# Performance work log

Hardware: AMD Instinct MI355X
Metric: run time of the kernel (lower is better)

## Reference

```python
import jax, jax.numpy as jnp
import numpy as np

EMBED_DIM = 1024
NUM_HEADS = 16
HEAD_DIM = EMBED_DIM // NUM_HEADS
LAMBDA_ENTANGLE = 0.35


def setup_inputs() -> dict:
    key = jax.random.key(0)
    ks = jax.random.split(key, 10)
    B, S, D = 2, 2048, EMBED_DIM
    init = 1.0 / np.sqrt(D)  # mimic nn.Linear uniform init scale
    x = jax.random.normal(ks[0], (B, S, D), dtype=jnp.float32)
    Wq = jax.random.uniform(ks[1], (D, D), jnp.float32, -init, init)
    bq = jax.random.uniform(ks[2], (D,), jnp.float32, -init, init)
    Wk = jax.random.uniform(ks[3], (D, D), jnp.float32, -init, init)
    bk = jax.random.uniform(ks[4], (D,), jnp.float32, -init, init)
    Wv = jax.random.uniform(ks[5], (D, D), jnp.float32, -init, init)
    bv = jax.random.uniform(ks[6], (D,), jnp.float32, -init, init)
    Wo = jax.random.uniform(ks[7], (D, D), jnp.float32, -init, init)
    bo = jax.random.uniform(ks[8], (D,), jnp.float32, -init, init)
    J_attn = jax.random.normal(ks[9], (NUM_HEADS, HEAD_DIM, HEAD_DIM), dtype=jnp.float32) * 0.02
    lambda_attn = jnp.asarray(LAMBDA_ENTANGLE, dtype=jnp.float32)
    return {"x": x, "Wq": Wq, "bq": bq, "Wk": Wk, "bk": bk, "Wv": Wv, "bv": bv,
            "Wo": Wo, "bo": bo, "J_attn": J_attn, "lambda_attn": lambda_attn}


def reference(x, Wq, bq, Wk, bk, Wv, bv, Wo, bo, J_attn, lambda_attn):
    B, S, D = x.shape
    H, Hd = NUM_HEADS, HEAD_DIM
    scale = jnp.sqrt(jnp.asarray(Hd, dtype=x.dtype))

    def heads(W, b):
        # (B,S,D) @ (D,D) + b -> (B,H,S,Hd)
        y = jnp.einsum('bsd,ed->bse', x, W) + b
        return y.reshape(B, S, H, Hd).transpose(0, 2, 1, 3)

    Q = heads(Wq, bq)
    K = heads(Wk, bk)
    V = heads(Wv, bv)

    scores = jnp.einsum('bhid,bhjd->bhij', Q, K) / scale
    # bilinear entanglement correction: tanh(Q) J tanh(K)^T
    QJ = jnp.einsum('bhid,hde->bhie', jnp.tanh(Q), J_attn)  # (B,H,S,Hd)
    delta = jnp.einsum('bhie,bhje->bhij', QJ, jnp.tanh(K))
    scores = scores + lambda_attn * delta

    causal = jnp.triu(jnp.ones((S, S), dtype=bool), k=1)
    scores = jnp.where(causal, -jnp.inf, scores)

    probs = jax.nn.softmax(scores, axis=-1)
    out = jnp.einsum('bhij,bhjd->bhid', probs, V)  # (B,H,S,Hd)
    out = out.transpose(0, 2, 1, 3).reshape(B, S, D)
    return jnp.einsum('bsd,ed->bse', out, Wo) + bo
```

## Files before the change

### kernel.cpp

```cpp
#include <hip/hip_runtime.h>
#include <hip/hip_bf16.h>

typedef unsigned short u16;
typedef __bf16 bf16x8 __attribute__((ext_vector_type(8)));
typedef float f32x4 __attribute__((ext_vector_type(4)));
typedef unsigned short u16x4 __attribute__((ext_vector_type(4)));

#define MFMA16(a, b, c) __builtin_amdgcn_mfma_f32_16x16x32_bf16(a, b, c, 0, 0, 0)

#define EMB 1024
#define SEQ 2048
#define NH 16
#define HD 64
#define LOG2E 1.4426950408889634f

#define GLOAD_LDS16(g, l) __builtin_amdgcn_global_load_lds( \
    (const __attribute__((address_space(1))) unsigned int*)(g), \
    (__attribute__((address_space(3))) unsigned int*)(l), 16, 0, 0)

__device__ __forceinline__ float b2f(u16 u) {
    union { unsigned int i; float f; } v; v.i = ((unsigned int)u) << 16; return v.f;
}
__device__ __forceinline__ u16 f2b(float f) {
    __hip_bfloat16 h = __float2bfloat16(f);
    return *reinterpret_cast<u16*>(&h);
}
__device__ __forceinline__ u16x4 pack4(float a, float b, float c, float d) {
    union { __hip_bfloat162 h2[2]; u16x4 u; } r;
    r.h2[0] = __float22bfloat162_rn(float2{a, b});
    r.h2[1] = __float22bfloat162_rn(float2{c, d});
    return r.u;
}
__device__ __forceinline__ bf16x8 ldfrag(const u16* p) {
    return *reinterpret_cast<const bf16x8*>(p);
}
__device__ __forceinline__ bf16x8 cvt8(const float* p) {
    const float4 a = *reinterpret_cast<const float4*>(p);
    const float4 b = *reinterpret_cast<const float4*>(p + 4);
    union { u16x4 q[2]; bf16x8 v; } r;
    r.q[0] = pack4(a.x, a.y, a.z, a.w);
    r.q[1] = pack4(b.x, b.y, b.z, b.w);
    return r.v;
}
__device__ __forceinline__ float fast_tanh(float x) {
    float t = __builtin_amdgcn_exp2f(x * (2.0f * LOG2E));
    return 1.0f - 2.0f * __builtin_amdgcn_rcpf(t + 1.0f);
}
__device__ __forceinline__ bf16x8 tanh8(bf16x8 v) {
    union { bf16x8 v; u16 u[8]; } in; in.v = v;
    float o[8];
#pragma unroll
    for (int e = 0; e < 8; e++) o[e] = fast_tanh(b2f(in.u[e]));
    union { u16x4 q[2]; bf16x8 v; } r;
    r.q[0] = pack4(o[0], o[1], o[2], o[3]);
    r.q[1] = pack4(o[4], o[5], o[6], o[7]);
    return r.v;
}

__global__ __launch_bounds__(256) void cvt_all(
        const float* __restrict__ x,  const float* __restrict__ Wq,
        const float* __restrict__ Wk, const float* __restrict__ Wv,
        const float* __restrict__ Wo, u16* __restrict__ dst)
{
    size_t i = ((size_t)blockIdx.x * 256 + threadIdx.x) * 8;
    const float* src; size_t off;
    if (i < 4194304) { src = x; off = i; }
    else {
        size_t j = i - 4194304; int w = (int)(j >> 20); off = j & 1048575;
        src = (w == 0) ? Wq : (w == 1) ? Wk : (w == 2) ? Wv : Wo;
    }
    *(bf16x8*)&dst[i] = cvt8(src + off);
}

template<int MI>
__global__ __launch_bounds__(256, 4) void gemm_epi(
        const u16* __restrict__ A,
        const u16* __restrict__ W0, const float* __restrict__ B0,
        const u16* __restrict__ W1, const float* __restrict__ B1,
        const u16* __restrict__ W2, const float* __restrict__ B2,
        const float* __restrict__ lam,
        u16* __restrict__ Qa, u16* __restrict__ Ka, u16* __restrict__ Vt,
        float* __restrict__ out, int modeBase)
{
    const int mode = modeBase + blockIdx.z;
    const u16* W; const float* bias;
    if (blockIdx.z == 0)      { W = W0; bias = B0; }
    else if (blockIdx.z == 1) { W = W1; bias = B1; }
    else                      { W = W2; bias = B2; }

    __shared__ __attribute__((aligned(16))) u16 sA[MI * 32 * 64];
    __shared__ __attribute__((aligned(16))) u16 sB[128 * 64];

    const int t = threadIdx.x;
    const int w = t >> 6, L = t & 63;
    const int wm = w >> 1, wn = w & 1;
    const int lr = L & 15, lq = L >> 4;
    const int wbase = t & 192;
    const int m0 = blockIdx.y * (MI * 32), n0 = blockIdx.x * 128;

    f32x4 acc[MI][4];
#pragma unroll
    for (int i = 0; i < MI; i++)
#pragma unroll
        for (int j = 0; j < 4; j++) { f32x4 z = {0.f, 0.f, 0.f, 0.f}; acc[i][j] = z; }

    for (int k0 = 0; k0 < EMB; k0 += 64) {
        __syncthreads();
#pragma unroll
        for (int q = 0; q < MI; q++) {
            int c = q * 256 + t;
            int row = c >> 3, cc = c & 7;
            int col8 = cc ^ (row & 7);
            GLOAD_LDS16(&A[(size_t)(m0 + row) * EMB + k0 + col8 * 8],
                        &sA[(q * 256 + wbase) * 8]);
        }
#pragma unroll
        for (int q = 0; q < 4; q++) {
            int c = q * 256 + t;
            int row = c >> 3, cc = c & 7;
            int col8 = cc ^ (row & 7);
            GLOAD_LDS16(&W[(size_t)(n0 + row) * EMB + k0 + col8 * 8],
                        &sB[(q * 256 + wbase) * 8]);
        }
        __syncthreads();
#pragma unroll
        for (int s = 0; s < 2; s++) {
            bf16x8 af[MI], bfr[4];
#pragma unroll
            for (int mi = 0; mi < MI; mi++) {
                int row = wm * (MI * 16) + mi * 16 + lr;
                af[mi] = ldfrag(&sA[(row * 8 + ((s * 4 + lq) ^ (row & 7))) * 8]);
            }
#pragma unroll
            for (int ni = 0; ni < 4; ni++) {
                int row = wn * 64 + ni * 16 + lr;
                bfr[ni] = ldfrag(&sB[(row * 8 + ((s * 4 + lq) ^ (row & 7))) * 8]);
            }
#pragma unroll
            for (int mi = 0; mi < MI; mi++)
#pragma unroll
                for (int ni = 0; ni < 4; ni++)
                    acc[mi][ni] = MFMA16(af[mi], bfr[ni], acc[mi][ni]);
        }
    }

    const float lamf = lam[0];
#pragma unroll
    for (int mi = 0; mi < MI; mi++)
#pragma unroll
        for (int ni = 0; ni < 4; ni++) {
            int mb = m0 + wm * (MI * 16) + mi * 16 + lq * 4;
            int n  = n0 + wn * 64 + ni * 16 + lr;
            float bv = bias[n];
            if (mode == 3) {
#pragma unroll
                for (int r = 0; r < 4; r++)
                    out[(size_t)(mb + r) * EMB + n] = acc[mi][ni][r] + bv;
            } else {
                int b = mb >> 11, s0 = mb & 2047;
                int h = n >> 6,  d = n & 63;
                if (mode == 0) {
#pragma unroll
                    for (int r = 0; r < 4; r++) {
                        float val = acc[mi][ni][r] + bv;
                        size_t i128 = ((size_t)(b * NH + h) * SEQ + s0 + r) * 128 + d;
                        Qa[i128]      = f2b(val * (0.125f * LOG2E));
                        Qa[i128 + 64] = f2b(lamf * LOG2E * fast_tanh(val));
                    }
                } else if (mode == 1) {
#pragma unroll
                    for (int r = 0; r < 4; r++) {
                        float val = acc[mi][ni][r] + bv;
                        Ka[((size_t)(b * NH + h) * SEQ + s0 + r) * 128 + d] = f2b(val);
                    }
                } else {
                    u16x4 pk = pack4(acc[mi][ni][0] + bv, acc[mi][ni][1] + bv,
                                     acc[mi][ni][2] + bv, acc[mi][ni][3] + bv);
                    *(u16x4*)&Vt[((size_t)(b * NH + h) * HD + d) * SEQ + s0] = pk;
                }
            }
        }
}

__global__ __launch_bounds__(256) void ukern(
        const float* __restrict__ J, u16* __restrict__ Ka)
{
    __shared__ __attribute__((aligned(16))) u16 sJ[64 * 72];
    const int t = threadIdx.x, w = t >> 6, L = t & 63, lr = L & 15, lq = L >> 4;
    const int rt = blockIdx.x, bh = blockIdx.y, h = bh & 15;

#pragma unroll
    for (int i = 0; i < 2; i++) {
        int c = t + 256 * i;
        int row = c >> 3, col = (c & 7) * 8;
        *(bf16x8*)&sJ[row * 72 + col] = cvt8(&J[(size_t)h * 4096 + row * 64 + col]);
    }
    __syncthreads();

    const u16* krow = &Ka[((size_t)bh * SEQ + rt * 64 + w * 16 + lr) * 128];
    bf16x8 a0 = tanh8(ldfrag(krow + lq * 8));
    bf16x8 a1 = tanh8(ldfrag(krow + lq * 8 + 32));
#pragma unroll
    for (int nt = 0; nt < 4; nt++) {
        f32x4 acc = {0.f, 0.f, 0.f, 0.f};
        acc = MFMA16(a0, ldfrag(&sJ[(nt * 16 + lr) * 72 + lq * 8]), acc);
        acc = MFMA16(a1, ldfrag(&sJ[(nt * 16 + lr) * 72 + lq * 8 + 32]), acc);
#pragma unroll
        for (int r = 0; r < 4; r++) {
            int j = rt * 64 + w * 16 + lq * 4 + r;
            Ka[((size_t)bh * SEQ + j) * 128 + 64 + nt * 16 + lr] = f2b(acc[r]);
        }
    }
}

__global__ __launch_bounds__(512) void flash(
        const u16* __restrict__ Qa, const u16* __restrict__ Ka,
        const u16* __restrict__ Vt, u16* __restrict__ attn)
{
    __shared__ __attribute__((aligned(16))) u16 sK[2][64 * 128];
    __shared__ __attribute__((aligned(16))) u16 sVt[2][64 * 64];
    __shared__ __attribute__((aligned(16))) u16 sP[128 * 72];
    __shared__ float sLs[2][4][64][2];

    const int t = threadIdx.x, w = t >> 6, L = t & 63, lr = L & 15, lq = L >> 4;
    const int wq = w & 3, wk = w >> 2;
    const int bh = blockIdx.x & 31, p = blockIdx.x >> 5;
    const int i_l = wq * 16 + lr;
    const u16* Kbase = Ka + (size_t)bh * SEQ * 128;
    const u16* Vbase = Vt + (size_t)bh * HD * SEQ;
    const int b = bh >> 4, h = bh & 15;
    float* sOt = reinterpret_cast<float*>(sK);

    const int kr0 = t >> 4,        kc0 = (t & 15) ^ (kr0 & 15);
    const int kr1 = (512 + t) >> 4, kc1 = (t & 15) ^ (kr1 & 15);
    const int vd = t >> 3,          vj8 = (t & 7) ^ (vd & 7);
    const u16* kq0 = Kbase + (size_t)kr0 * 128 + kc0 * 8;
    const u16* kq1 = Kbase + (size_t)kr1 * 128 + kc1 * 8;
    const u16* vq  = Vbase + (size_t)vd * SEQ + vj8 * 8;

#pragma unroll 1
    for (int seg = 0; seg < 2; seg++) {
        const int qt = seg ? 15 - p : p;
        const int qm = qt * 128;
        const int ktmax = 2 * qt + 1;

        bf16x8 qf[2][4];
#pragma unroll
        for (int g = 0; g < 2; g++) {
            const u16* qrow = Qa + ((size_t)bh * SEQ + qm + g * 64 + i_l) * 128;
#pragma unroll
            for (int s = 0; s < 4; s++) qf[g][s] = ldfrag(qrow + s * 32 + lq * 8);
        }

        f32x4 Ot[2][4];
#pragma unroll
        for (int g = 0; g < 2; g++)
#pragma unroll
            for (int i = 0; i < 4; i++) { f32x4 z = {0.f, 0.f, 0.f, 0.f}; Ot[g][i] = z; }
        float lsum[2] = {0.f, 0.f};

        {
            int4 rk0 = *(const int4*)kq0;
            int4 rk1 = *(const int4*)kq1;
            int4 rv  = *(const int4*)vq;
            *(int4*)&sK[0][(size_t)t * 8]         = rk0;
            *(int4*)&sK[0][(size_t)(512 + t) * 8] = rk1;
            *(int4*)&sVt[0][(size_t)t * 8]        = rv;
        }
        __syncthreads();

        int cur = 0;
        for (int kt = 0; kt <= ktmax; kt++) {
            const bool pf = kt < ktmax;
            int4 rk0, rk1, rv;
            if (pf) {
                const int kn = (kt + 1) * 64;
                rk0 = *(const int4*)(kq0 + (size_t)kn * 128);
                rk1 = *(const int4*)(kq1 + (size_t)kn * 128);
                rv  = *(const int4*)(vq + kn);
            }
            const u16* sKc = sK[cur];
            const u16* sVc = sVt[cur];

            f32x4 sc[2][2];
#pragma unroll
            for (int g = 0; g < 2; g++)
#pragma unroll
                for (int m = 0; m < 2; m++) { f32x4 z = {0.f,0.f,0.f,0.f}; sc[g][m] = z; }
            __builtin_amdgcn_s_setprio(1);
#pragma unroll
            for (int mt2 = 0; mt2 < 2; mt2++) {
                int j = (wk * 2 + mt2) * 16 + lr;
#pragma unroll
                for (int s = 0; s < 4; s++) {
                    bf16x8 kf = ldfrag(&sKc[(j * 16 + ((s * 4 + lq) ^ (j & 15))) * 8]);
                    sc[0][mt2] = MFMA16(kf, qf[0][s], sc[0][mt2]);
                    sc[1][mt2] = MFMA16(kf, qf[1][s], sc[1][mt2]);
                }
            }
            __builtin_amdgcn_s_setprio(0);
            if (kt >= ktmax - 1) {
                const int thr0 = (kt == ktmax) ? -1  : i_l;
                const int thr1 = (kt == ktmax) ? i_l : 63;
#pragma unroll
                for (int mt2 = 0; mt2 < 2; mt2++)
#pragma unroll
                    for (int r = 0; r < 4; r++) {
                        int j = (wk * 2 + mt2) * 16 + lq * 4 + r;
                        if (j > thr0) sc[0][mt2][r] = -INFINITY;
                        if (j > thr1) sc[1][mt2][r] = -INFINITY;
                    }
            }
#pragma unroll
            for (int g = 0; g < 2; g++) {
#pragma unroll
                for (int mt2 = 0; mt2 < 2; mt2++) {
                    float e0 = __builtin_amdgcn_exp2f(sc[g][mt2][0]);
                    float e1 = __builtin_amdgcn_exp2f(sc[g][mt2][1]);
                    float e2 = __builtin_amdgcn_exp2f(sc[g][mt2][2]);
                    float e3 = __builtin_amdgcn_exp2f(sc[g][mt2][3]);
                    lsum[g] += (e0 + e1) + (e2 + e3);
                    *(u16x4*)&sP[(g * 64 + i_l) * 72 + (wk * 2 + mt2) * 16 + lq * 4] =
                        pack4(e0, e1, e2, e3);
                }
            }
            __builtin_amdgcn_s_setprio(1);
            {
                bf16x8 pf0 = ldfrag(&sP[(i_l) * 72 + wk * 32 + lq * 8]);
                bf16x8 pf1 = ldfrag(&sP[(64 + i_l) * 72 + wk * 32 + lq * 8]);
#pragma unroll
                for (int mt = 0; mt < 4; mt++) {
                    int d = mt * 16 + lr;
                    bf16x8 vf = ldfrag(&sVc[(d * 8 + ((wk * 4 + lq) ^ (d & 7))) * 8]);
                    Ot[0][mt] = MFMA16(vf, pf0, Ot[0][mt]);
                    Ot[1][mt] = MFMA16(vf, pf1, Ot[1][mt]);
                }
            }
            __builtin_amdgcn_s_setprio(0);
            if (pf) {
                *(int4*)&sK[cur ^ 1][(size_t)t * 8]         = rk0;
                *(int4*)&sK[cur ^ 1][(size_t)(512 + t) * 8] = rk1;
                *(int4*)&sVt[cur ^ 1][(size_t)t * 8]        = rv;
            }
            __syncthreads();
            cur ^= 1;
        }

#pragma unroll
        for (int g = 0; g < 2; g++) {
            lsum[g] += __shfl_xor(lsum[g], 16);
            lsum[g] += __shfl_xor(lsum[g], 32);
            sLs[wk][wq][L][g] = lsum[g];
        }
        if (wk == 1) {
            float* dst = &sOt[wq * 64 + L];
#pragma unroll
            for (int g = 0; g < 2; g++)
#pragma unroll
                for (int mt = 0; mt < 4; mt++)
#pragma unroll
                    for (int r = 0; r < 4; r++)
                        dst[256 * (g * 16 + mt * 4 + r)] = Ot[g][mt][r];
        }
        __syncthreads();
        if (wk == 0) {
            const float* src = &sOt[wq * 64 + L];
#pragma unroll
            for (int g = 0; g < 2; g++) {
                float ls = lsum[g] + sLs[1][wq][L][g];
                const float r0 = __builtin_amdgcn_rcpf(ls);
                const float inv = r0 * (2.0f - ls * r0);
                const size_t base =
                    ((size_t)(b * SEQ + qm + g * 64 + i_l)) * EMB + h * HD;
#pragma unroll
                for (int mt = 0; mt < 4; mt++)
                    *(u16x4*)&attn[base + mt * 16 + lq * 4] = pack4(
                        (Ot[g][mt][0] + src[256 * (g * 16 + mt * 4 + 0)]) * inv,
                        (Ot[g][mt][1] + src[256 * (g * 16 + mt * 4 + 1)]) * inv,
                        (Ot[g][mt][2] + src[256 * (g * 16 + mt * 4 + 2)]) * inv,
                        (Ot[g][mt][3] + src[256 * (g * 16 + mt * 4 + 3)]) * inv);
            }
        }
        __syncthreads();
    }
}

extern "C" void kernel_launch(void* const* d_in, const int* in_sizes, int n_in,
                              void* d_out, int out_size, void* d_ws, size_t ws_size,
                              hipStream_t stream)
{
    const float* x   = (const float*)d_in[0];
    const float* Wq  = (const float*)d_in[1];
    const float* bq  = (const float*)d_in[2];
    const float* Wk  = (const float*)d_in[3];
    const float* bk  = (const float*)d_in[4];
    const float* Wv  = (const float*)d_in[5];
    const float* bv  = (const float*)d_in[6];
    const float* Wo  = (const float*)d_in[7];
    const float* bo  = (const float*)d_in[8];
    const float* J   = (const float*)d_in[9];
    const float* lam = (const float*)d_in[10];

    u16* ws  = (u16*)d_ws;
    u16* xb  = ws;
    u16* Wqb = xb  + (size_t)4096 * 1024;
    u16* Wkb = Wqb + (size_t)1024 * 1024;
    u16* Wvb = Wkb + (size_t)1024 * 1024;
    u16* Wob = Wvb + (size_t)1024 * 1024;
    u16* Qa  = Wob + (size_t)1024 * 1024;
    u16* Ka  = Qa  + (size_t)32 * 2048 * 128;
    u16* Vt  = Ka  + (size_t)32 * 2048 * 128;
    u16* attn = xb;
    float* dout = (float*)d_out;

    dim3 blk(256);
    cvt_all<<<dim3(4096), blk, 0, stream>>>(x, Wq, Wk, Wv, Wo, ws);
    gemm_epi<4><<<dim3(8, 32, 3), blk, 0, stream>>>(
        xb, Wqb, bq, Wkb, bk, Wvb, bv, lam, Qa, Ka, Vt, dout, 0);
    ukern<<<dim3(32, 32), blk, 0, stream>>>(J, Ka);
    flash<<<dim3(256), dim3(512), 0, stream>>>(Qa, Ka, Vt, attn);
    gemm_epi<2><<<dim3(8, 64, 1), blk, 0, stream>>>(
        attn, Wob, bo, Wob, bo, Wob, bo, lam, Qa, Ka, Vt, dout, 3);
}
```

Before: 190.8 us.

## Fuse tanh(K)·J into K projection epilogue and enlarge flash KV tile

The separate ukern launch is removed. The K-projection GEMM epilogue now stages tanh(K) in its shared memory and multiplies it by a bf16 copy of J, which cvt_all now produces. Separately, the flash attention kernel's key/value tile grows from 64 to 128 columns, halving loop iterations and barriers, and the causal masking logic is simplified to match. The cost is much larger LDS use in flash (double-buffered 128-row K/V plus a wider P tile), which may lower occupancy, and an extra barrier plus MFMA work in the K GEMM blocks.

```diff
diff --git a/kernel.cpp b/kernel.cpp
--- a/kernel.cpp
+++ b/kernel.cpp
@@ -46,30 +46,24 @@
     float t = __builtin_amdgcn_exp2f(x * (2.0f * LOG2E));
     return 1.0f - 2.0f * __builtin_amdgcn_rcpf(t + 1.0f);
 }
-__device__ __forceinline__ bf16x8 tanh8(bf16x8 v) {
-    union { bf16x8 v; u16 u[8]; } in; in.v = v;
-    float o[8];
-#pragma unroll
-    for (int e = 0; e < 8; e++) o[e] = fast_tanh(b2f(in.u[e]));
-    union { u16x4 q[2]; bf16x8 v; } r;
-    r.q[0] = pack4(o[0], o[1], o[2], o[3]);
-    r.q[1] = pack4(o[4], o[5], o[6], o[7]);
-    return r.v;
-}
 
 __global__ __launch_bounds__(256) void cvt_all(
         const float* __restrict__ x,  const float* __restrict__ Wq,
         const float* __restrict__ Wk, const float* __restrict__ Wv,
-        const float* __restrict__ Wo, u16* __restrict__ dst)
+        const float* __restrict__ Wo, const float* __restrict__ J,
+        u16* __restrict__ dst)
 {
     size_t i = ((size_t)blockIdx.x * 256 + threadIdx.x) * 8;
-    const float* src; size_t off;
-    if (i < 4194304) { src = x; off = i; }
-    else {
+    const float* src; size_t off; u16* d;
+    if (i < 4194304) { src = x; off = i; d = dst + i; }
+    else if (i < 8388608) {
         size_t j = i - 4194304; int w = (int)(j >> 20); off = j & 1048575;
         src = (w == 0) ? Wq : (w == 1) ? Wk : (w == 2) ? Wv : Wo;
-    }
-    *(bf16x8*)&dst[i] = cvt8(src + off);
+        d = dst + i;
+    } else {
+        off = i - 8388608; src = J; d = dst + 29360128 + off;
+    }
+    *(bf16x8*)d = cvt8(src + off);
 }
 
 template<int MI>
@@ -78,7 +72,7 @@
         const u16* __restrict__ W0, const float* __restrict__ B0,
         const u16* __restrict__ W1, const float* __restrict__ B1,
         const u16* __restrict__ W2, const float* __restrict__ B2,
-        const float* __restrict__ lam,
+        const float* __restrict__ lam, const u16* __restrict__ Jb,
         u16* __restrict__ Qa, u16* __restrict__ Ka, u16* __restrict__ Vt,
         float* __restrict__ out, int modeBase)
 {
@@ -144,6 +138,9 @@
         }
     }
 
+    if (mode == 1) __syncthreads();
+    u16* sU = (w < 2) ? &sA[(size_t)w * 4096] : &sB[(size_t)(w - 2) * 4096];
+
     const float lamf = lam[0];
 #pragma unroll
     for (int mi = 0; mi < MI; mi++)
@@ -172,6 +169,9 @@
                     for (int r = 0; r < 4; r++) {
                         float val = acc[mi][ni][r] + bv;
                         Ka[((size_t)(b * NH + h) * SEQ + s0 + r) * 128 + d] = f2b(val);
+                        int row64 = mi * 16 + lq * 4 + r;
+                        int phys = (d >> 3) ^ (row64 & 7);
+                        sU[row64 * 64 + phys * 8 + (d & 7)] = f2b(fast_tanh(val));
                     }
                 } else {
                     u16x4 pk = pack4(acc[mi][ni][0] + bv, acc[mi][ni][1] + bv,
@@ -180,35 +180,34 @@
                 }
             }
         }
-}
-
-__global__ __launch_bounds__(256) void ukern(
-        const float* __restrict__ J, u16* __restrict__ Ka)
-{
-    __shared__ __attribute__((aligned(16))) u16 sJ[64 * 72];
-    const int t = threadIdx.x, w = t >> 6, L = t & 63, lr = L & 15, lq = L >> 4;
-    const int rt = blockIdx.x, bh = blockIdx.y, h = bh & 15;
-
-#pragma unroll
-    for (int i = 0; i < 2; i++) {
-        int c = t + 256 * i;
-        int row = c >> 3, col = (c & 7) * 8;
-        *(bf16x8*)&sJ[row * 72 + col] = cvt8(&J[(size_t)h * 4096 + row * 64 + col]);
-    }
-    __syncthreads();
-
-    const u16* krow = &Ka[((size_t)bh * SEQ + rt * 64 + w * 16 + lr) * 128];
-    bf16x8 a0 = tanh8(ldfrag(krow + lq * 8));
-    bf16x8 a1 = tanh8(ldfrag(krow + lq * 8 + 32));
-#pragma unroll
-    for (int nt = 0; nt < 4; nt++) {
-        f32x4 acc = {0.f, 0.f, 0.f, 0.f};
-        acc = MFMA16(a0, ldfrag(&sJ[(nt * 16 + lr) * 72 + lq * 8]), acc);
-        acc = MFMA16(a1, ldfrag(&sJ[(nt * 16 + lr) * 72 + lq * 8 + 32]), acc);
-#pragma unroll
-        for (int r = 0; r < 4; r++) {
-            int j = rt * 64 + w * 16 + lq * 4 + r;
-            Ka[((size_t)bh * SEQ + j) * 128 + 64 + nt * 16 + lr] = f2b(acc[r]);
+
+    if (mode == 1) {
+        const int hn = (n0 >> 6) + wn;
+        const u16* Jh = Jb + (size_t)hn * 4096;
+        bf16x8 jf[4][2];
+#pragma unroll
+        for (int nt = 0; nt < 4; nt++)
+#pragma unroll
+            for (int s2 = 0; s2 < 2; s2++)
+                jf[nt][s2] = ldfrag(&Jh[(nt * 16 + lr) * 64 + s2 * 32 + lq * 8]);
+#pragma unroll
+        for (int rt2 = 0; rt2 < 4; rt2++) {
+            int r64 = rt2 * 16 + lr;
+            bf16x8 a0 = ldfrag(&sU[r64 * 64 + ((0 + lq) ^ (r64 & 7)) * 8]);
+            bf16x8 a1 = ldfrag(&sU[r64 * 64 + ((4 + lq) ^ (r64 & 7)) * 8]);
+#pragma unroll
+            for (int nt = 0; nt < 4; nt++) {
+                f32x4 acc2 = {0.f, 0.f, 0.f, 0.f};
+                acc2 = MFMA16(a0, jf[nt][0], acc2);
+                acc2 = MFMA16(a1, jf[nt][1], acc2);
+#pragma unroll
+                for (int r = 0; r < 4; r++) {
+                    int grow = m0 + wm * 64 + rt2 * 16 + lq * 4 + r;
+                    int bb = grow >> 11, ss = grow & 2047;
+                    Ka[((size_t)(bb * NH + hn) * SEQ + ss) * 128 + 64 + nt * 16 + lr]
+                        = f2b(acc2[r]);
+                }
+            }
         }
     }
 }
@@ -217,9 +216,9 @@
         const u16* __restrict__ Qa, const u16* __restrict__ Ka,
         const u16* __restrict__ Vt, u16* __restrict__ attn)
 {
-    __shared__ __attribute__((aligned(16))) u16 sK[2][64 * 128];
-    __shared__ __attribute__((aligned(16))) u16 sVt[2][64 * 64];
-    __shared__ __attribute__((aligned(16))) u16 sP[128 * 72];
+    __shared__ __attribute__((aligned(16))) u16 sK[2][128 * 128];
+    __shared__ __attribute__((aligned(16))) u16 sVt[2][64 * 128];
+    __shared__ __attribute__((aligned(16))) u16 sP[128 * 136];
     __shared__ float sLs[2][4][64][2];
 
     const int t = threadIdx.x, w = t >> 6, L = t & 63, lr = L & 15, lq = L >> 4;
@@ -231,18 +230,25 @@
     const int b = bh >> 4, h = bh & 15;
     float* sOt = reinterpret_cast<float*>(sK);
 
-    const int kr0 = t >> 4,        kc0 = (t & 15) ^ (kr0 & 15);
-    const int kr1 = (512 + t) >> 4, kc1 = (t & 15) ^ (kr1 & 15);
-    const int vd = t >> 3,          vj8 = (t & 7) ^ (vd & 7);
-    const u16* kq0 = Kbase + (size_t)kr0 * 128 + kc0 * 8;
-    const u16* kq1 = Kbase + (size_t)kr1 * 128 + kc1 * 8;
-    const u16* vq  = Vbase + (size_t)vd * SEQ + vj8 * 8;
+    const u16* kq[4];
+#pragma unroll
+    for (int q = 0; q < 4; q++) {
+        int c = q * 512 + t;
+        int row = c >> 4, cc = c & 15;
+        kq[q] = Kbase + (size_t)row * 128 + (cc ^ (row & 15)) * 8;
+    }
+    const u16* vq[2];
+#pragma unroll
+    for (int q = 0; q < 2; q++) {
+        int c = q * 512 + t;
+        int d = c >> 4, cc = c & 15;
+        vq[q] = Vbase + (size_t)d * SEQ + (cc ^ (d & 7)) * 8;
+    }
 
 #pragma unroll 1
     for (int seg = 0; seg < 2; seg++) {
         const int qt = seg ? 15 - p : p;
         const int qm = qt * 128;
-        const int ktmax = 2 * qt + 1;
 
         bf16x8 qf[2][4];
 #pragma unroll
@@ -260,37 +266,46 @@
         float lsum[2] = {0.f, 0.f};
 
         {
-            int4 rk0 = *(const int4*)kq0;
-            int4 rk1 = *(const int4*)kq1;
-            int4 rv  = *(const int4*)vq;
-            *(int4*)&sK[0][(size_t)t * 8]         = rk0;
-            *(int4*)&sK[0][(size_t)(512 + t) * 8] = rk1;
-            *(int4*)&sVt[0][(size_t)t * 8]        = rv;
+            int4 a0 = *(const int4*)kq[0];
+            int4 a1 = *(const int4*)kq[1];
+            int4 a2 = *(const int4*)kq[2];
+            int4 a3 = *(const int4*)kq[3];
+            int4 b0 = *(const int4*)vq[0];
+            int4 b1 = *(const int4*)vq[1];
+            *(int4*)&sK[0][(size_t)(0 * 512 + t) * 8] = a0;
+            *(int4*)&sK[0][(size_t)(1 * 512 + t) * 8] = a1;
+            *(int4*)&sK[0][(size_t)(2 * 512 + t) * 8] = a2;
+            *(int4*)&sK[0][(size_t)(3 * 512 + t) * 8] = a3;
+            *(int4*)&sVt[0][(size_t)(0 * 512 + t) * 8] = b0;
+            *(int4*)&sVt[0][(size_t)(1 * 512 + t) * 8] = b1;
         }
         __syncthreads();
 
         int cur = 0;
-        for (int kt = 0; kt <= ktmax; kt++) {
-            const bool pf = kt < ktmax;
-            int4 rk0, rk1, rv;
+        for (int kt = 0; kt <= qt; kt++) {
+            const bool pf = kt < qt;
+            int4 rk0, rk1, rk2, rk3, rv0, rv1;
             if (pf) {
-                const int kn = (kt + 1) * 64;
-                rk0 = *(const int4*)(kq0 + (size_t)kn * 128);
-                rk1 = *(const int4*)(kq1 + (size_t)kn * 128);
-                rv  = *(const int4*)(vq + kn);
+                const int kn = (kt + 1) * 128;
+                rk0 = *(const int4*)(kq[0] + (size_t)kn * 128);
+                rk1 = *(const int4*)(kq[1] + (size_t)kn * 128);
+                rk2 = *(const int4*)(kq[2] + (size_t)kn * 128);
+                rk3 = *(const int4*)(kq[3] + (size_t)kn * 128);
+                rv0 = *(const int4*)(vq[0] + kn);
+                rv1 = *(const int4*)(vq[1] + kn);
             }
             const u16* sKc = sK[cur];
             const u16* sVc = sVt[cur];
 
-            f32x4 sc[2][2];
+            f32x4 sc[2][4];
 #pragma unroll
             for (int g = 0; g < 2; g++)
 #pragma unroll
-                for (int m = 0; m < 2; m++) { f32x4 z = {0.f,0.f,0.f,0.f}; sc[g][m] = z; }
+                for (int m = 0; m < 4; m++) { f32x4 z = {0.f,0.f,0.f,0.f}; sc[g][m] = z; }
             __builtin_amdgcn_s_setprio(1);
 #pragma unroll
-            for (int mt2 = 0; mt2 < 2; mt2++) {
-                int j = (wk * 2 + mt2) * 16 + lr;
+            for (int mt2 = 0; mt2 < 4; mt2++) {
+                int j = wk * 64 + mt2 * 16 + lr;
 #pragma unroll
                 for (int s = 0; s < 4; s++) {
                     bf16x8 kf = ldfrag(&sKc[(j * 16 + ((s * 4 + lq) ^ (j & 15))) * 8]);
@@ -299,48 +314,51 @@
                 }
             }
             __builtin_amdgcn_s_setprio(0);
-            if (kt >= ktmax - 1) {
-                const int thr0 = (kt == ktmax) ? -1  : i_l;
-                const int thr1 = (kt == ktmax) ? i_l : 63;
-#pragma unroll
-                for (int mt2 = 0; mt2 < 2; mt2++)
+            if (kt == qt) {
+#pragma unroll
+                for (int mt2 = 0; mt2 < 4; mt2++)
 #pragma unroll
                     for (int r = 0; r < 4; r++) {
-                        int j = (wk * 2 + mt2) * 16 + lq * 4 + r;
-                        if (j > thr0) sc[0][mt2][r] = -INFINITY;
-                        if (j > thr1) sc[1][mt2][r] = -INFINITY;
+                        int jj = wk * 64 + mt2 * 16 + lq * 4 + r;
+                        if (jj > i_l)      sc[0][mt2][r] = -INFINITY;
+                        if (jj > 64 + i_l) sc[1][mt2][r] = -INFINITY;
                     }
             }
 #pragma unroll
             for (int g = 0; g < 2; g++) {
 #pragma unroll
-                for (int mt2 = 0; mt2 < 2; mt2++) {
+                for (int mt2 = 0; mt2 < 4; mt2++) {
                     float e0 = __builtin_amdgcn_exp2f(sc[g][mt2][0]);
                     float e1 = __builtin_amdgcn_exp2f(sc[g][mt2][1]);
                     float e2 = __builtin_amdgcn_exp2f(sc[g][mt2][2]);
                     float e3 = __builtin_amdgcn_exp2f(sc[g][mt2][3]);
                     lsum[g] += (e0 + e1) + (e2 + e3);
-                    *(u16x4*)&sP[(g * 64 + i_l) * 72 + (wk * 2 + mt2) * 16 + lq * 4] =
+                    *(u16x4*)&sP[(g * 64 + i_l) * 136 + wk * 64 + mt2 * 16 + lq * 4] =
                         pack4(e0, e1, e2, e3);
                 }
             }
             __builtin_amdgcn_s_setprio(1);
-            {
-                bf16x8 pf0 = ldfrag(&sP[(i_l) * 72 + wk * 32 + lq * 8]);
-                bf16x8 pf1 = ldfrag(&sP[(64 + i_l) * 72 + wk * 32 + lq * 8]);
+#pragma unroll
+            for (int s2l = 0; s2l < 2; s2l++) {
+                bf16x8 pf0 = ldfrag(&sP[(i_l) * 136 + wk * 64 + s2l * 32 + lq * 8]);
+                bf16x8 pf1 = ldfrag(&sP[(64 + i_l) * 136 + wk * 64 + s2l * 32 + lq * 8]);
 #pragma unroll
                 for (int mt = 0; mt < 4; mt++) {
                     int d = mt * 16 + lr;
-                    bf16x8 vf = ldfrag(&sVc[(d * 8 + ((wk * 4 + lq) ^ (d & 7))) * 8]);
+                    bf16x8 vf = ldfrag(
+                        &sVc[(d * 16 + ((wk * 8 + s2l * 4 + lq) ^ (d & 7))) * 8]);
                     Ot[0][mt] = MFMA16(vf, pf0, Ot[0][mt]);
                     Ot[1][mt] = MFMA16(vf, pf1, Ot[1][mt]);
                 }
             }
             __builtin_amdgcn_s_setprio(0);
             if (pf) {
-                *(int4*)&sK[cur ^ 1][(size_t)t * 8]         = rk0;
-                *(int4*)&sK[cur ^ 1][(size_t)(512 + t) * 8] = rk1;
-                *(int4*)&sVt[cur ^ 1][(size_t)t * 8]        = rv;
+                *(int4*)&sK[cur ^ 1][(size_t)(0 * 512 + t) * 8] = rk0;
+                *(int4*)&sK[cur ^ 1][(size_t)(1 * 512 + t) * 8] = rk1;
+                *(int4*)&sK[cur ^ 1][(size_t)(2 * 512 + t) * 8] = rk2;
+                *(int4*)&sK[cur ^ 1][(size_t)(3 * 512 + t) * 8] = rk3;
+                *(int4*)&sVt[cur ^ 1][(size_t)(0 * 512 + t) * 8] = rv0;
+                *(int4*)&sVt[cur ^ 1][(size_t)(1 * 512 + t) * 8] = rv1;
             }
             __syncthreads();
             cur ^= 1;
@@ -410,15 +428,15 @@
     u16* Qa  = Wob + (size_t)1024 * 1024;
     u16* Ka  = Qa  + (size_t)32 * 2048 * 128;
     u16* Vt  = Ka  + (size_t)32 * 2048 * 128;
+    u16* Jb  = Vt  + (size_t)32 * 64 * 2048;
     u16* attn = xb;
     float* dout = (float*)d_out;
 
     dim3 blk(256);
-    cvt_all<<<dim3(4096), blk, 0, stream>>>(x, Wq, Wk, Wv, Wo, ws);
+    cvt_all<<<dim3(4128), blk, 0, stream>>>(x, Wq, Wk, Wv, Wo, J, ws);
     gemm_epi<4><<<dim3(8, 32, 3), blk, 0, stream>>>(
-        xb, Wqb, bq, Wkb, bk, Wvb, bv, lam, Qa, Ka, Vt, dout, 0);
-    ukern<<<dim3(32, 32), blk, 0, stream>>>(J, Ka);
+        xb, Wqb, bq, Wkb, bk, Wvb, bv, lam, Jb, Qa, Ka, Vt, dout, 0);
     flash<<<dim3(256), dim3(512), 0, stream>>>(Qa, Ka, Vt, attn);
     gemm_epi<2><<<dim3(8, 64, 1), blk, 0, stream>>>(
-        attn, Wob, bo, Wob, bo, Wob, bo, lam, Qa, Ka, Vt, dout, 3);
-}
+        attn, Wob, bo, Wob, bo, Wob, bo, lam, Jb, Qa, Ka, Vt, dout, 3);
+}
```

After: 186.1 us. -2.5%, faster.
